# Kernel optimization log

Measured on AMD Instinct MI355X. Metric: run time of the kernel, lower is better.

The kernel has to match this reference:

```python
import jax, jax.numpy as jnp
import numpy as np

MD = 4                  # corr_md
D = 2 * MD + 1          # patch_size = 9


def setup_inputs() -> dict:
    key = jax.random.key(0)
    k1, k2 = jax.random.split(key)
    b, c, h, w = 4, 128, 128, 256
    t1 = jax.random.normal(k1, (b, c, h, w), dtype=jnp.float32)
    t2 = jax.random.normal(k2, (b, c, h, w), dtype=jnp.float32)
    return {"t1": t1, "t2": t2}


def reference(t1, t2):
    # Local cost volume: for each displacement (di, dj) in [-MD, MD]^2,
    # out[b, p, y, x] = sum_c t1[b, c, y, x] * t2[b, c, y+di, x+dj]
    # with zero padding outside t2 (SpatialCorrelationSampler semantics,
    # kernel_size=1, stride=1, dilation_patch=1; no channel normalization).
    b, c, h, w = t1.shape
    t2p = jnp.pad(t2, ((0, 0), (0, 0), (MD, MD), (MD, MD)))
    # Loop over the fixed 9x9 displacement grid (81 small reductions);
    outs = [
        jnp.einsum('bchw,bchw->bhw', t1, t2p[:, :, i:i + h, j:j + w])
        for i in range(D) for j in range(D)
    ]
    return jnp.stack(outs, axis=1)  # [b, 81, h, w]
```

## Files before the change

### kernel.cpp

```cpp
#include <hip/hip_runtime.h>

#define NP 81
#define CC 128
#define HH 128
#define WW 256
#define YP 136
#define XP 288
#define WS_NEED 40108032ull

typedef __attribute__((ext_vector_type(8))) short short8;
typedef __attribute__((ext_vector_type(4))) float f32x4;
typedef __attribute__((ext_vector_type(16))) float f32x16;

__device__ __forceinline__ short f2bf(float f) {
    unsigned int u = __builtin_bit_cast(unsigned int, f);
    u += 0x7fffu + ((u >> 16) & 1u);
    return (short)(u >> 16);
}

__global__ __launch_bounds__(256) void prepass_t2(const float* __restrict__ t2,
                                                  short* __restrict__ ws) {
    const int u = blockIdx.x * 256 + threadIdx.x;
    const int xp = u % XP;
    const int v  = u / XP;
    const int yp = v % YP;
    const int bc = v / YP;
    const int y2 = yp - 4, x2 = xp - 4;
    short8 lo = {0,0,0,0,0,0,0,0}, hi = {0,0,0,0,0,0,0,0};
    if (y2 >= 0 && y2 < HH && x2 >= 0 && x2 < WW) {
        const int b = bc >> 3, cg = bc & 7;
        const size_t pl = (size_t)HH * WW;
        const float* p = t2 + ((size_t)(b * CC + cg * 16) * HH + y2) * WW + x2;
#pragma unroll
        for (int j = 0; j < 8; j++) lo[j] = f2bf(p[(size_t)j * pl]);
#pragma unroll
        for (int j = 0; j < 8; j++) hi[j] = f2bf(p[(size_t)(j + 8) * pl]);
    }
    short* o = ws + (size_t)u * 16;
    *(short8*)o = lo;
    *(short8*)(o + 8) = hi;
}

__global__ __launch_bounds__(576) void corr32_kernel(const float* __restrict__ t1,
                                                     const short* __restrict__ ws,
                                                     float* __restrict__ out) {
    const int id = blockIdx.x;
    const int xt = id & 7;
    const int y  = (id >> 3) & (HH - 1);
    const int b  = id >> 10;
    const int X0 = xt * 32;

    const int tid  = threadIdx.x;
    const int lane = tid & 63;
    const int w    = tid >> 6;
    const int n    = lane & 31;
    const int g    = lane >> 5;

    __shared__ short smem[4608 + 9216];
    short* sA = smem;
    short* sB = smem + 4608;

    const size_t plane = (size_t)HH * WW;

    if (tid < 512) {
        const int x = tid & 31, oct = tid >> 5;
        const float* p = t1 + (size_t)(b * CC + oct * 8) * plane
                       + (size_t)y * WW + X0 + x;
        short8 pk;
#pragma unroll
        for (int j = 0; j < 8; j++) pk[j] = f2bf(p[(size_t)j * plane]);
        *(short8*)&sA[x * 144 + oct * 8] = pk;
    }

    f32x16 accv[2];
#pragma unroll
    for (int t = 0; t < 2; ++t)
#pragma unroll
        for (int r = 0; r < 16; ++r) accv[t][r] = 0.f;

    const int u0 = tid, u1 = tid + 576;
    const int r0 = u0 >> 7, s0 = u0 & 127;
    const int r1 = u1 >> 7, s1 = u1 & 127;
    const size_t base0 = ((size_t)b * 8 * YP + (y + r0)) * XP + X0;
    const size_t base1 = ((size_t)b * 8 * YP + (y + r1)) * XP + X0;

    short8 pf0 = *(const short8*)(ws + base0 * 16 + s0 * 8);
    short8 pf1 = *(const short8*)(ws + base1 * 16 + s1 * 8);

    for (int kc = 0; kc < 8; ++kc) {
        __syncthreads();
        *(short8*)&sB[r0 * 1024 + s0 * 8] = pf0;
        *(short8*)&sB[r1 * 1024 + s1 * 8] = pf1;
        if (kc < 7) {
            const size_t adv = (size_t)(kc + 1) * YP * XP * 16;
            pf0 = *(const short8*)(ws + base0 * 16 + adv + s0 * 8);
            pf1 = *(const short8*)(ws + base1 * 16 + adv + s1 * 8);
        }
        __syncthreads();
        const short8 af  = *(const short8*)&sA[n * 144 + kc * 16 + g * 8];
        const short8 bf0 = *(const short8*)&sB[w * 1024 + n * 16 + g * 8];
        const short8 bf1 = *(const short8*)&sB[w * 1024 + (32 + n) * 16 + g * 8];
        accv[0] = __builtin_amdgcn_mfma_f32_32x32x16_bf16(af, bf0, accv[0], 0, 0, 0);
        accv[1] = __builtin_amdgcn_mfma_f32_32x32x16_bf16(af, bf1, accv[1], 0, 0, 0);
    }

    __syncthreads();
    float* obuf = (float*)smem;
#pragma unroll
    for (int t = 0; t < 2; ++t)
#pragma unroll
        for (int r = 0; r < 16; ++r) {
            const int m  = (r & 3) + 8 * (r >> 2) + 4 * g;
            const int dj = n - m + 32 * t;
            if (dj >= 0 && dj <= 8) obuf[(w * 9 + dj) * 40 + m] = accv[t][r];
        }
    __syncthreads();
    for (int u = tid; u < 648; u += 576) {
        const int p = u >> 3, xq = u & 7;
        f32x4 v = *(const f32x4*)&obuf[p * 40 + xq * 4];
        *(f32x4*)&out[((size_t)(b * NP + p) * HH + y) * WW + X0 + xq * 4] = v;
    }
}

__global__ __launch_bounds__(256) void corr_mfma_kernel(
        const float* __restrict__ t1, const float* __restrict__ t2,
        float* __restrict__ out) {
    const int id = blockIdx.x;
    const int xt = id & 3;
    const int y  = (id >> 2) & (HH - 1);
    const int b  = id >> 9;
    const int X0 = xt * 64;
    const int tid  = threadIdx.x;
    const int lane = tid & 63;
    const int wv   = tid >> 6;
    const int n    = lane & 15;
    const int q    = lane >> 4;
    __shared__ short smem[2560 + 28800];
    short* sA = smem;
    short* sB = smem + 2560;
    f32x4 acc[9][2];
#pragma unroll
    for (int i = 0; i < 9; i++)
#pragma unroll
        for (int t = 0; t < 2; t++) acc[i][t] = (f32x4){0.f, 0.f, 0.f, 0.f};
    const size_t plane = (size_t)HH * WW;
    const float* t1b = t1 + (size_t)b * CC * plane + (size_t)y * WW;
    const float* t2b = t2 + (size_t)b * CC * plane;
    for (int c0 = 0; c0 < CC; c0 += 32) {
        __syncthreads();
        {
            const int x  = tid & 63;
            const int cg = tid >> 6;
            const float* p = t1b + (size_t)(c0 + cg * 8) * plane + X0 + x;
            short8 pk;
#pragma unroll
            for (int j = 0; j < 8; j++) pk[j] = f2bf(p[(size_t)j * plane]);
            *(short8*)&sA[x * 40 + cg * 8] = pk;
        }
#pragma unroll
        for (int i = 0; i < 12; i++) {
            const int u = tid + i * 256;
            if (u < 2880) {
                const int r   = u / 320;
                const int rem = u - r * 320;
                const int cg  = rem / 80;
                const int ix  = rem - cg * 80;
                const int y2  = y + r - 4;
                const int x2  = X0 - 4 + ix;
                short8 pk;
                if (y2 >= 0 && y2 < HH && x2 >= 0 && x2 < WW) {
                    const float* p = t2b + (size_t)(c0 + cg * 8) * plane
                                   + (size_t)y2 * WW + x2;
#pragma unroll
                    for (int j = 0; j < 8; j++) pk[j] = f2bf(p[(size_t)j * plane]);
                } else {
#pragma unroll
                    for (int j = 0; j < 8; j++) pk[j] = 0;
                }
                *(short8*)&sB[r * 3200 + ix * 40 + cg * 8] = pk;
            }
        }
        __syncthreads();
        const short8 af = *(const short8*)&sA[(16 * wv + n) * 40 + q * 8];
#pragma unroll
        for (int di = 0; di < 9; di++) {
#pragma unroll
            for (int t = 0; t < 2; t++) {
                const short8 bf = *(const short8*)
                    &sB[di * 3200 + (16 * wv + 16 * t + n) * 40 + q * 8];
                acc[di][t] = __builtin_amdgcn_mfma_f32_16x16x32_bf16(
                    af, bf, acc[di][t], 0, 0, 0);
            }
        }
    }
    __syncthreads();
    float* obuf = (float*)smem;
#pragma unroll
    for (int di = 0; di < 9; di++)
#pragma unroll
        for (int t = 0; t < 2; t++)
#pragma unroll
            for (int r = 0; r < 4; r++) {
                const int m  = q * 4 + r;
                const int dj = n - m + 16 * t;
                if (dj >= 0 && dj <= 8)
                    obuf[(di * 9 + dj) * 68 + 16 * wv + m] = acc[di][t][r];
            }
    __syncthreads();
    float* ob = out + (size_t)b * NP * plane + (size_t)y * WW + X0;
#pragma unroll
    for (int i = 0; i < 6; i++) {
        const int u = tid + i * 256;
        if (u < 1296) {
            const int p  = u >> 4;
            const int xu = u & 15;
            f32x4 v = *(const f32x4*)&obuf[p * 68 + xu * 4];
            *(f32x4*)&ob[(size_t)p * plane + xu * 4] = v;
        }
    }
}

extern "C" void kernel_launch(void* const* d_in, const int* in_sizes, int n_in,
                              void* d_out, int out_size, void* d_ws, size_t ws_size,
                              hipStream_t stream) {
    const float* t1 = (const float*)d_in[0];
    const float* t2 = (const float*)d_in[1];
    float* out = (float*)d_out;
    if (ws_size >= WS_NEED) {
        short* ws = (short*)d_ws;
        prepass_t2<<<4896, 256, 0, stream>>>(t2, ws);
        corr32_kernel<<<4096, 576, 0, stream>>>(t1, ws, out);
    } else {
        corr_mfma_kernel<<<2048, 256, 0, stream>>>(t1, t2, out);
    }
}
```

Baseline: 205.8 us.

## Load B fragments directly from workspace into registers, drop LDS staging and barriers

The correlation kernel no longer stages the t2 slab in shared memory. Each lane loads its MFMA B fragments straight from the pre-packed bf16 workspace with a one-step register prefetch, which removes two barriers per channel chunk. The t1 tile in LDS now uses an XOR swizzle instead of padding, shared memory shrinks, and launch bounds request 7 blocks per CU for more occupancy. The risk is that overlapping rows are now read from global or L2 memory by several waves rather than once, and the loads are less coalesced.

```diff
diff --git a/kernel.cpp b/kernel.cpp
--- a/kernel.cpp
+++ b/kernel.cpp
@@ -41,9 +41,9 @@
     *(short8*)(o + 8) = hi;
 }
 
-__global__ __launch_bounds__(576) void corr32_kernel(const float* __restrict__ t1,
-                                                     const short* __restrict__ ws,
-                                                     float* __restrict__ out) {
+__global__ __launch_bounds__(576, 7) void corr32_v2(const float* __restrict__ t1,
+                                                    const short* __restrict__ ws,
+                                                    float* __restrict__ out) {
     const int id = blockIdx.x;
     const int xt = id & 7;
     const int y  = (id >> 3) & (HH - 1);
@@ -56,9 +56,8 @@
     const int n    = lane & 31;
     const int g    = lane >> 5;
 
-    __shared__ short smem[4608 + 9216];
-    short* sA = smem;
-    short* sB = smem + 4608;
+    __shared__ float smemf[3240];
+    short* sA = (short*)smemf;
 
     const size_t plane = (size_t)HH * WW;
 
@@ -69,50 +68,46 @@
         short8 pk;
 #pragma unroll
         for (int j = 0; j < 8; j++) pk[j] = f2bf(p[(size_t)j * plane]);
-        *(short8*)&sA[x * 144 + oct * 8] = pk;
-    }
-
-    f32x16 accv[2];
+        *(short8*)&sA[x * 128 + ((oct ^ (x & 15)) * 8)] = pk;
+    }
+
+    f32x16 acc[2];
 #pragma unroll
     for (int t = 0; t < 2; ++t)
 #pragma unroll
-        for (int r = 0; r < 16; ++r) accv[t][r] = 0.f;
-
-    const int u0 = tid, u1 = tid + 576;
-    const int r0 = u0 >> 7, s0 = u0 & 127;
-    const int r1 = u1 >> 7, s1 = u1 & 127;
-    const size_t base0 = ((size_t)b * 8 * YP + (y + r0)) * XP + X0;
-    const size_t base1 = ((size_t)b * 8 * YP + (y + r1)) * XP + X0;
-
-    short8 pf0 = *(const short8*)(ws + base0 * 16 + s0 * 8);
-    short8 pf1 = *(const short8*)(ws + base1 * 16 + s1 * 8);
-
+        for (int r = 0; r < 16; ++r) acc[t][r] = 0.f;
+
+    const size_t cstride = (size_t)YP * XP * 16;
+    size_t bofs = ((((size_t)b * 8) * YP + (y + w)) * XP + (X0 + n)) * 16 + g * 8;
+
+    short8 c0 = *(const short8*)(ws + bofs);
+    short8 c1 = *(const short8*)(ws + bofs + 512);
+
+    __syncthreads();
+
+#pragma unroll
     for (int kc = 0; kc < 8; ++kc) {
-        __syncthreads();
-        *(short8*)&sB[r0 * 1024 + s0 * 8] = pf0;
-        *(short8*)&sB[r1 * 1024 + s1 * 8] = pf1;
+        short8 p0, p1;
         if (kc < 7) {
-            const size_t adv = (size_t)(kc + 1) * YP * XP * 16;
-            pf0 = *(const short8*)(ws + base0 * 16 + adv + s0 * 8);
-            pf1 = *(const short8*)(ws + base1 * 16 + adv + s1 * 8);
-        }
-        __syncthreads();
-        const short8 af  = *(const short8*)&sA[n * 144 + kc * 16 + g * 8];
-        const short8 bf0 = *(const short8*)&sB[w * 1024 + n * 16 + g * 8];
-        const short8 bf1 = *(const short8*)&sB[w * 1024 + (32 + n) * 16 + g * 8];
-        accv[0] = __builtin_amdgcn_mfma_f32_32x32x16_bf16(af, bf0, accv[0], 0, 0, 0);
-        accv[1] = __builtin_amdgcn_mfma_f32_32x32x16_bf16(af, bf1, accv[1], 0, 0, 0);
-    }
-
-    __syncthreads();
-    float* obuf = (float*)smem;
+            p0 = *(const short8*)(ws + bofs + cstride);
+            p1 = *(const short8*)(ws + bofs + cstride + 512);
+        }
+        const short8 af = *(const short8*)
+            &sA[n * 128 + (((kc * 2 + g) ^ (n & 15)) * 8)];
+        acc[0] = __builtin_amdgcn_mfma_f32_32x32x16_bf16(af, c0, acc[0], 0, 0, 0);
+        acc[1] = __builtin_amdgcn_mfma_f32_32x32x16_bf16(af, c1, acc[1], 0, 0, 0);
+        if (kc < 7) { c0 = p0; c1 = p1; bofs += cstride; }
+    }
+
+    __syncthreads();
+    float* obuf = smemf;
 #pragma unroll
     for (int t = 0; t < 2; ++t)
 #pragma unroll
         for (int r = 0; r < 16; ++r) {
             const int m  = (r & 3) + 8 * (r >> 2) + 4 * g;
             const int dj = n - m + 32 * t;
-            if (dj >= 0 && dj <= 8) obuf[(w * 9 + dj) * 40 + m] = accv[t][r];
+            if (dj >= 0 && dj <= 8) obuf[(w * 9 + dj) * 40 + m] = acc[t][r];
         }
     __syncthreads();
     for (int u = tid; u < 648; u += 576) {
@@ -229,7 +224,7 @@
     if (ws_size >= WS_NEED) {
         short* ws = (short*)d_ws;
         prepass_t2<<<4896, 256, 0, stream>>>(t2, ws);
-        corr32_kernel<<<4096, 576, 0, stream>>>(t1, ws, out);
+        corr32_v2<<<4096, 576, 0, stream>>>(t1, ws, out);
     } else {
         corr_mfma_kernel<<<2048, 256, 0, stream>>>(t1, t2, out);
     }
```

Measured after the change: 196.4 us. 4.6% less time.
